# Optimization experiments

Hardware: AMD Instinct MI355X
Metric: run time of the kernel (lower is better)

## Reference

```python
import jax, jax.numpy as jnp
import numpy as np

HEADS = 8
DIM_HEAD = 64
DIM = 512
KERNEL = 33
SCALE = DIM_HEAD ** -0.5


def setup_inputs() -> dict:
    key = jax.random.key(0)
    k1, k2, k3, k4, k5, k6 = jax.random.split(key, 6)
    b, n = 2, 2048
    inner = HEADS * DIM_HEAD
    x = jax.random.normal(k1, (b, n, DIM), dtype=jnp.float32)
    mask = jax.random.uniform(k2, (b, n)) < 0.9
    W_qkv = jax.random.normal(k3, (DIM, inner * 3), dtype=jnp.float32) / np.sqrt(DIM)
    W_out = jax.random.normal(k4, (inner, DIM), dtype=jnp.float32) / np.sqrt(inner)
    b_out = jax.random.normal(k5, (DIM,), dtype=jnp.float32) * 0.01
    # depthwise Conv2d(heads, heads, (K,1), groups=heads) weight: (O=heads, I/groups=1, K, 1)
    conv_w = jax.random.normal(k6, (HEADS, 1, KERNEL, 1), dtype=jnp.float32) / np.sqrt(KERNEL)
    return {"x": x, "mask": mask, "W_qkv": W_qkv, "W_out": W_out,
            "b_out": b_out, "conv_w": conv_w}


def reference(x, mask, W_qkv, W_out, b_out, conv_w):
    b, n, _ = x.shape
    h, d = HEADS, DIM_HEAD
    qkv = (x @ W_qkv).reshape(b, n, 3, h, d)          # chunk(3) then (h d) split
    q = qkv[:, :, 0].transpose(0, 2, 1, 3)            # b h n d
    k = qkv[:, :, 1].transpose(0, 2, 1, 3)
    v = qkv[:, :, 2].transpose(0, 2, 1, 3)
    dots = jnp.einsum('bhid,bhjd->bhij', q, k) * SCALE
    mask_value = -jnp.finfo(dots.dtype).max
    dots = jnp.where(mask[:, None, None, :], dots, mask_value)
    attn = jax.nn.softmax(dots, axis=-1)
    out = jnp.einsum('bhij,bhjd->bhid', attn, v)      # b h n d
    # depthwise residual conv over sequence axis (height), per head
    pad = KERNEL // 2
    res = jax.lax.conv_general_dilated(
        v, conv_w, window_strides=(1, 1), padding=((pad, pad), (0, 0)),
        dimension_numbers=('NCHW', 'OIHW', 'NCHW'), feature_group_count=h)
    out = out + res
    out = out.transpose(0, 2, 1, 3).reshape(b, n, h * d)  # b n (h d)
    out = out @ W_out + b_out
    out = jnp.where(mask[:, :, None], out, 0.0)
    return out
```

## Files before the change

### kernel.cpp

```cpp
#include <hip/hip_runtime.h>
#include <float.h>

#define BATCH 2
#define SEQ   2048
#define HEADS 8
#define DHEAD 64
#define DIMM  512
#define NQKV  1536
#define QK_SCALE 0.125f

#define QKV_ELEMS ((size_t)BATCH * HEADS * SEQ * DHEAD)

typedef __bf16 bf16x8 __attribute__((ext_vector_type(8)));
typedef float  f32x4  __attribute__((ext_vector_type(4)));

__device__ __forceinline__ unsigned short bfbits(float f) {
  __bf16 h = (__bf16)f;
  return *(unsigned short*)&h;
}
__device__ __forceinline__ float bf2f(unsigned short u) {
  return __uint_as_float((unsigned)u << 16);
}

__global__ __launch_bounds__(1024) void prep_mask(const void* __restrict__ mraw,
                                                  float* __restrict__ maskf) {
  __shared__ int f_bf16, f_f32, f_gt1, f_oddnz;
  const int t = threadIdx.x;
  if (t == 0) { f_bf16 = 0; f_f32 = 0; f_gt1 = 0; f_oddnz = 0; }
  __syncthreads();
  const unsigned int* w = (const unsigned int*)mraw;
  unsigned int v = w[t];
  if (v == 0x3f803f80u) f_bf16 = 1;
  if (v == 0x3f800000u) f_f32 = 1;
  if (v > 1u)           f_gt1 = 1;
  if ((t & 1) && v != 0u) f_oddnz = 1;
  __syncthreads();
  int mode;
  if (f_bf16)       mode = 4;
  else if (f_f32)   mode = 3;
  else if (f_gt1)   mode = 1;
  else if (!f_oddnz) mode = 2;
  else              mode = 0;
  for (int i = t; i < BATCH * SEQ; i += 1024) {
    bool keep;
    if (mode == 4)      keep = ((const unsigned short*)mraw)[i] != 0;
    else if (mode == 3) keep = ((const float*)mraw)[i] != 0.f;
    else if (mode == 1) keep = ((const unsigned char*)mraw)[i] != 0;
    else if (mode == 2) keep = w[2 * i] != 0u;
    else                keep = w[i] != 0u;
    maskf[i] = keep ? 1.f : 0.f;
  }
}

__global__ __launch_bounds__(256) void transpose_w(const float* __restrict__ W,
                                                   unsigned short* __restrict__ Wt,
                                                   int K, int N) {
  __shared__ float T[64][65];
  const int t = threadIdx.x;
  const int n0 = blockIdx.x * 64, k0 = blockIdx.y * 64;
  {
    int r0 = t >> 4, c4 = t & 15;
#pragma unroll
    for (int rr = 0; rr < 4; ++rr) {
      int r = r0 + rr * 16;
      float4 v = *(const float4*)(W + (size_t)(k0 + r) * N + n0 + c4 * 4);
      T[r][c4 * 4 + 0] = v.x; T[r][c4 * 4 + 1] = v.y;
      T[r][c4 * 4 + 2] = v.z; T[r][c4 * 4 + 3] = v.w;
    }
  }
  __syncthreads();
  {
    int n = t >> 2, kc = t & 3;
    union { unsigned short u[16]; int4 v[2]; } p;
#pragma unroll
    for (int i = 0; i < 16; ++i) p.u[i] = bfbits(T[kc * 16 + i][n]);
    int4* dst = (int4*)(Wt + (size_t)(n0 + n) * K + k0 + kc * 16);
    dst[0] = p.v[0]; dst[1] = p.v[1];
  }
}

__global__ __launch_bounds__(256) void gemm_qkv_mfma(
    const float* __restrict__ X, const unsigned short* __restrict__ Wt,
    unsigned short* __restrict__ Qbf, unsigned short* __restrict__ Kbf,
    unsigned short* __restrict__ Vt) {
  __shared__ __align__(16) unsigned char Al[128 * 128];
  __shared__ __align__(16) unsigned char Bl[64 * 128];
  const int tid = threadIdx.x;
  const int lane = tid & 63;
  const int w = tid >> 6;
  const int l15 = lane & 15, g = lane >> 4;
  const int wr = w >> 1, wc = w & 1;
  int bid = blockIdx.x;
  int lid = (bid & 7) * 96 + (bid >> 3);
  int by = lid / 24, bx = lid - by * 24;
  const int m0 = by * 128;

  f32x4 acc[4][2] = {};
  const int srow = tid >> 3, scg = tid & 7;
  const int rsw = (l15 & 7) << 4;

  for (int k0 = 0; k0 < DIMM; k0 += 64) {
    __syncthreads();
#pragma unroll
    for (int it = 0; it < 4; ++it) {
      int row = srow + it * 32;
      int sw = (row & 7) << 4;
      const float* asrc = X + (size_t)(m0 + row) * DIMM + k0 + scg * 8;
      float4 a0 = *(const float4*)asrc;
      float4 a1 = *(const float4*)(asrc + 4);
      union { unsigned short u[8]; int4 v; } pk;
      pk.u[0] = bfbits(a0.x); pk.u[1] = bfbits(a0.y);
      pk.u[2] = bfbits(a0.z); pk.u[3] = bfbits(a0.w);
      pk.u[4] = bfbits(a1.x); pk.u[5] = bfbits(a1.y);
      pk.u[6] = bfbits(a1.z); pk.u[7] = bfbits(a1.w);
      *(int4*)(Al + row * 128 + ((scg * 16) ^ sw)) = pk.v;
      if (it < 2) {
        *(int4*)(Bl + row * 128 + ((scg * 16) ^ sw)) =
            *(const int4*)(Wt + (size_t)(bx * 64 + row) * DIMM + k0 + scg * 8);
      }
    }
    __syncthreads();
#pragma unroll
    for (int ks = 0; ks < 2; ++ks) {
      bf16x8 af[4], bfr[2];
#pragma unroll
      for (int mi = 0; mi < 4; ++mi)
        af[mi] = *(const bf16x8*)(Al + (wr * 64 + mi * 16 + l15) * 128 +
                                  ((ks * 64 + g * 16) ^ rsw));
#pragma unroll
      for (int nj = 0; nj < 2; ++nj)
        bfr[nj] = *(const bf16x8*)(Bl + (wc * 32 + nj * 16 + l15) * 128 +
                                   ((ks * 64 + g * 16) ^ rsw));
#pragma unroll
      for (int mi = 0; mi < 4; ++mi)
#pragma unroll
        for (int nj = 0; nj < 2; ++nj)
          acc[mi][nj] = __builtin_amdgcn_mfma_f32_16x16x32_bf16(
              af[mi], bfr[nj], acc[mi][nj], 0, 0, 0);
    }
  }
  const int chunk = bx >> 3;
  const int bb = m0 >> 11;
#pragma unroll
  for (int nj = 0; nj < 2; ++nj) {
    int col = (bx & 7) * 64 + wc * 32 + nj * 16 + l15;
    int hh = col >> 6, dd = col & 63;
#pragma unroll
    for (int mi = 0; mi < 4; ++mi) {
      int ii0 = (m0 & (SEQ - 1)) + wr * 64 + mi * 16 + g * 4;
      if (chunk == 2) {
        union { unsigned short u[4]; ushort4 v; } pk;
#pragma unroll
        for (int r = 0; r < 4; ++r) pk.u[r] = bfbits(acc[mi][nj][r]);
        *(ushort4*)(Vt + ((size_t)(bb * HEADS + hh) * DHEAD + dd) * SEQ + ii0) = pk.v;
      } else {
        unsigned short* dst = (chunk == 0) ? Qbf : Kbf;
        float sc = (chunk == 0) ? QK_SCALE : 1.f;
#pragma unroll
        for (int r = 0; r < 4; ++r)
          dst[((size_t)(bb * HEADS + hh) * SEQ + ii0 + r) * DHEAD + dd] =
              bfbits(acc[mi][nj][r] * sc);
      }
    }
  }
}

__global__ __launch_bounds__(256) void attn_split(const unsigned short* __restrict__ Qbf,
                                                  const unsigned short* __restrict__ Kbf,
                                                  const unsigned short* __restrict__ Vt,
                                                  const float* __restrict__ maskf,
                                                  unsigned short* __restrict__ Po,
                                                  float* __restrict__ LSE) {
  __shared__ __align__(16) unsigned char Ks[8192];
  __shared__ __align__(16) unsigned char Vs[8192];
  __shared__ __align__(16) unsigned char Ps[8192];
  __shared__ float skm[64];

  const int tid = threadIdx.x;
  const int lane = tid & 63;
  const int w = tid >> 6;
  const int l15 = lane & 15, g = lane >> 4;

  int fid = blockIdx.x;
  int lid = (fid & 7) * 128 + (fid >> 3);
  const int bh = lid >> 6;
  const int rem = lid & 63;
  const int qb = rem >> 1;
  const int half = rem & 1;
  const int bb = bh >> 3;

  const unsigned short* Qg = Qbf + ((size_t)bh * SEQ + qb * 64) * DHEAD;
  const unsigned short* Kg = Kbf + (size_t)bh * SEQ * DHEAD;
  const unsigned short* Vg = Vt  + (size_t)bh * DHEAD * SEQ;

  bf16x8 qf0, qf1;
  {
    const unsigned char* qrow = (const unsigned char*)(Qg + (size_t)(w * 16 + l15) * DHEAD);
    qf0 = *(const bf16x8*)(qrow + g * 16);
    qf1 = *(const bf16x8*)(qrow + 64 + g * 16);
  }

  f32x4 o[4];
  float mrow[4], lrow[4];
#pragma unroll
  for (int j = 0; j < 4; ++j) { o[j] = (f32x4){0.f, 0.f, 0.f, 0.f}; }
#pragma unroll
  for (int r = 0; r < 4; ++r) { mrow[r] = -3.0e38f; lrow[r] = 0.f; }

  const int sm = tid >> 2;
  const int sc = (tid & 3) * 32;
  const int ssw = (sm & 7) << 4;
  const int rsw = (l15 & 7) << 4;

  const int kt0 = half * 16;
  for (int kt = kt0; kt < kt0 + 16; ++kt) {
    __syncthreads();
    {
      const unsigned char* ksrc =
          (const unsigned char*)(Kg + (size_t)kt * 64 * DHEAD) + sm * 128 + sc;
      const unsigned char* vsrc =
          (const unsigned char*)(Vg + (size_t)sm * SEQ + kt * 64) + sc;
      *(int4*)(Ks + sm * 128 + ((sc)      ^ ssw)) = *(const int4*)(ksrc);
      *(int4*)(Ks + sm * 128 + ((sc + 16) ^ ssw)) = *(const int4*)(ksrc + 16);
      *(int4*)(Vs + sm * 128 + ((sc)      ^ ssw)) = *(const int4*)(vsrc);
      *(int4*)(Vs + sm * 128 + ((sc + 16) ^ ssw)) = *(const int4*)(vsrc + 16);
      if (tid < 64) skm[tid] = maskf[bb * SEQ + kt * 64 + tid];
    }
    __syncthreads();

    f32x4 s[4];
#pragma unroll
    for (int j = 0; j < 4; ++j) {
      const unsigned char* krow = Ks + (16 * j + l15) * 128;
      bf16x8 kf0 = *(const bf16x8*)(krow + ((g * 16)      ^ rsw));
      bf16x8 kf1 = *(const bf16x8*)(krow + ((64 + g * 16) ^ rsw));
      f32x4 z = (f32x4){0.f, 0.f, 0.f, 0.f};
      z = __builtin_amdgcn_mfma_f32_16x16x32_bf16(qf0, kf0, z, 0, 0, 0);
      z = __builtin_amdgcn_mfma_f32_16x16x32_bf16(qf1, kf1, z, 0, 0, 0);
      s[j] = z;
    }

    float km0 = skm[l15], km1 = skm[16 + l15], km2 = skm[32 + l15], km3 = skm[48 + l15];
#pragma unroll
    for (int r = 0; r < 4; ++r) {
      float v0 = (km0 != 0.f) ? s[0][r] : -1e30f;
      float v1 = (km1 != 0.f) ? s[1][r] : -1e30f;
      float v2 = (km2 != 0.f) ? s[2][r] : -1e30f;
      float v3 = (km3 != 0.f) ? s[3][r] : -1e30f;
      float rm = fmaxf(fmaxf(v0, v1), fmaxf(v2, v3));
      rm = fmaxf(rm, __shfl_xor(rm, 1));
      rm = fmaxf(rm, __shfl_xor(rm, 2));
      rm = fmaxf(rm, __shfl_xor(rm, 4));
      rm = fmaxf(rm, __shfl_xor(rm, 8));
      float mnew = fmaxf(mrow[r], rm);
      float resc = __expf(mrow[r] - mnew);
      float p0 = __expf(v0 - mnew) * km0;
      float p1 = __expf(v1 - mnew) * km1;
      float p2 = __expf(v2 - mnew) * km2;
      float p3 = __expf(v3 - mnew) * km3;
      float rs = (p0 + p1) + (p2 + p3);
      rs += __shfl_xor(rs, 1);
      rs += __shfl_xor(rs, 2);
      rs += __shfl_xor(rs, 4);
      rs += __shfl_xor(rs, 8);
      lrow[r] = lrow[r] * resc + rs;
      mrow[r] = mnew;
      o[0][r] *= resc; o[1][r] *= resc; o[2][r] *= resc; o[3][r] *= resc;

      int pm = w * 16 + g * 4 + r;
      unsigned char* prow = Ps + pm * 128;
      int psw = (pm & 7) << 4;
      *(__bf16*)(prow + ((2 * (l15)      ) ^ psw)) = (__bf16)p0;
      *(__bf16*)(prow + ((2 * (16 + l15) ) ^ psw)) = (__bf16)p1;
      *(__bf16*)(prow + ((2 * (32 + l15) ) ^ psw)) = (__bf16)p2;
      *(__bf16*)(prow + ((2 * (48 + l15) ) ^ psw)) = (__bf16)p3;
    }

    {
      const unsigned char* parow = Ps + (w * 16 + l15) * 128;
      bf16x8 pa0 = *(const bf16x8*)(parow + ((g * 16)      ^ rsw));
      bf16x8 pa1 = *(const bf16x8*)(parow + ((64 + g * 16) ^ rsw));
#pragma unroll
      for (int j = 0; j < 4; ++j) {
        const unsigned char* vrow = Vs + (16 * j + l15) * 128;
        bf16x8 vf0 = *(const bf16x8*)(vrow + ((g * 16)      ^ rsw));
        bf16x8 vf1 = *(const bf16x8*)(vrow + ((64 + g * 16) ^ rsw));
        o[j] = __builtin_amdgcn_mfma_f32_16x16x32_bf16(pa0, vf0, o[j], 0, 0, 0);
        o[j] = __builtin_amdgcn_mfma_f32_16x16x32_bf16(pa1, vf1, o[j], 0, 0, 0);
      }
    }
  }

#pragma unroll
  for (int r = 0; r < 4; ++r) {
    float l = lrow[r];
    float inv = (l > 0.f) ? 1.f / l : 0.f;
    int row = qb * 64 + w * 16 + g * 4 + r;
    size_t base = half * QKV_ELEMS + ((size_t)bh * SEQ + row) * DHEAD + l15;
    Po[base]      = bfbits(o[0][r] * inv);
    Po[base + 16] = bfbits(o[1][r] * inv);
    Po[base + 32] = bfbits(o[2][r] * inv);
    Po[base + 48] = bfbits(o[3][r] * inv);
    if (l15 == 0)
      LSE[half * (BATCH * HEADS * SEQ) + bh * SEQ + row] =
          (l > 0.f) ? mrow[r] + __logf(l) : -3.0e38f;
  }
}

__global__ __launch_bounds__(256) void combine_conv(
    const unsigned short* __restrict__ Po, const float* __restrict__ LSE,
    const unsigned short* __restrict__ Vt, const float* __restrict__ cw,
    unsigned short* __restrict__ Obf) {
  __shared__ float T[96][68];
  __shared__ float cwl[33];
  const int tid = threadIdx.x;
  const int bid = blockIdx.x;
  const int bh = bid >> 5;
  const int n0 = (bid & 31) * 64;
  const int hh = bh & 7;
  if (tid < 33) cwl[tid] = cw[hh * 33 + tid];
  for (int idx = tid; idx < 64 * 24; idx += 256) {
    int d = idx / 24, c4 = idx - (idx / 24) * 24;
    int nbase = n0 - 16 + c4 * 4;
    const unsigned short* src = Vt + ((size_t)bh * DHEAD + d) * SEQ;
#pragma unroll
    for (int q = 0; q < 4; ++q) {
      int n = nbase + q;
      T[c4 * 4 + q][d] = (n >= 0 && n < SEQ) ? bf2f(src[n]) : 0.f;
    }
  }
  __syncthreads();
#pragma unroll
  for (int p = 0; p < 4; ++p) {
    int n = (tid >> 4) + p * 16;
    int d4 = tid & 15;
    int row = bh * SEQ + n0 + n;
    float ls0 = LSE[row], ls1 = LSE[BATCH * HEADS * SEQ + row];
    float m = fmaxf(ls0, ls1);
    float w0 = __expf(ls0 - m), w1 = __expf(ls1 - m);
    float inv = 1.f / (w0 + w1);
    w0 *= inv; w1 *= inv;
    const unsigned short* p0 = Po + (size_t)row * DHEAD + d4 * 4;
    const unsigned short* p1 = p0 + QKV_ELEMS;
    ushort4 a = *(const ushort4*)p0, b = *(const ushort4*)p1;
    float o0 = w0 * bf2f(a.x) + w1 * bf2f(b.x);
    float o1 = w0 * bf2f(a.y) + w1 * bf2f(b.y);
    float o2 = w0 * bf2f(a.z) + w1 * bf2f(b.z);
    float o3 = w0 * bf2f(a.w) + w1 * bf2f(b.w);
#pragma unroll
    for (int t = 0; t < 33; ++t) {
      float wv = cwl[t];
      float4 tv = *(const float4*)&T[n + t][d4 * 4];
      o0 += wv * tv.x; o1 += wv * tv.y; o2 += wv * tv.z; o3 += wv * tv.w;
    }
    union { unsigned short u[4]; ushort4 v; } pk;
    pk.u[0] = bfbits(o0); pk.u[1] = bfbits(o1);
    pk.u[2] = bfbits(o2); pk.u[3] = bfbits(o3);
    *(ushort4*)(Obf + (size_t)row * DHEAD + d4 * 4) = pk.v;
  }
}

__global__ __launch_bounds__(256) void gemm_out_mfma(
    const unsigned short* __restrict__ Obf, const unsigned short* __restrict__ Wt,
    const float* __restrict__ bias, const float* __restrict__ maskf,
    float* __restrict__ out) {
  __shared__ __align__(16) unsigned char Al[64 * 128];
  __shared__ __align__(16) unsigned char Bl[64 * 128];
  const int tid = threadIdx.x;
  const int lane = tid & 63;
  const int w = tid >> 6;
  const int l15 = lane & 15, g = lane >> 4;
  const int wr = w >> 1, wc = w & 1;
  int bid = blockIdx.x;
  int lid = (bid & 7) * 64 + (bid >> 3);
  int by = lid >> 3, bx = lid & 7;
  const int m0 = by * 64, n0 = bx * 64;
  const int bb = m0 >> 11;
  const int ii0 = m0 & (SEQ - 1);

  f32x4 acc[2][2] = {};
  const int srow = tid >> 3, scg = tid & 7;
  const int rsw = (l15 & 7) << 4;

  for (int k0 = 0; k0 < DIMM; k0 += 64) {
    const int hh = k0 >> 6;
    __syncthreads();
#pragma unroll
    for (int it = 0; it < 2; ++it) {
      int row = srow + it * 32;
      int sw = (row & 7) << 4;
      *(int4*)(Al + row * 128 + ((scg * 16) ^ sw)) =
          *(const int4*)(Obf + ((size_t)(bb * HEADS + hh) * SEQ + ii0 + row) * DHEAD + scg * 8);
      *(int4*)(Bl + row * 128 + ((scg * 16) ^ sw)) =
          *(const int4*)(Wt + (size_t)(n0 + row) * DIMM + k0 + scg * 8);
    }
    __syncthreads();
#pragma unroll
    for (int ks = 0; ks < 2; ++ks) {
      bf16x8 af[2], bfr[2];
#pragma unroll
      for (int mi = 0; mi < 2; ++mi)
        af[mi] = *(const bf16x8*)(Al + (wr * 32 + mi * 16 + l15) * 128 +
                                  ((ks * 64 + g * 16) ^ rsw));
#pragma unroll
      for (int nj = 0; nj < 2; ++nj)
        bfr[nj] = *(const bf16x8*)(Bl + (wc * 32 + nj * 16 + l15) * 128 +
                                   ((ks * 64 + g * 16) ^ rsw));
#pragma unroll
      for (int mi = 0; mi < 2; ++mi)
#pragma unroll
        for (int nj = 0; nj < 2; ++nj)
          acc[mi][nj] = __builtin_amdgcn_mfma_f32_16x16x32_bf16(
              af[mi], bfr[nj], acc[mi][nj], 0, 0, 0);
    }
  }
#pragma unroll
  for (int nj = 0; nj < 2; ++nj) {
    int col = n0 + wc * 32 + nj * 16 + l15;
    float bcol = bias[col];
#pragma unroll
    for (int mi = 0; mi < 2; ++mi) {
#pragma unroll
      for (int r = 0; r < 4; ++r) {
        int m = m0 + wr * 32 + mi * 16 + g * 4 + r;
        out[(size_t)m * DIMM + col] = (acc[mi][nj][r] + bcol) * maskf[m];
      }
    }
  }
}

extern "C" void kernel_launch(void* const* d_in, const int* in_sizes, int n_in,
                              void* d_out, int out_size, void* d_ws, size_t ws_size,
                              hipStream_t stream) {
  const float* x     = (const float*)d_in[0];
  const void*  mask  = d_in[1];
  const float* Wqkv  = (const float*)d_in[2];
  const float* Wout  = (const float*)d_in[3];
  const float* bout  = (const float*)d_in[4];
  const float* convw = (const float*)d_in[5];
  float* out = (float*)d_out;

  float* maskf = (float*)d_ws;
  unsigned short* Qbf = (unsigned short*)(maskf + 4096);
  unsigned short* Kbf = Qbf + QKV_ELEMS;
  unsigned short* Vt  = Kbf + QKV_ELEMS;
  unsigned short* Po  = Vt + QKV_ELEMS;
  float* LSE          = (float*)(Po + 2 * QKV_ELEMS);
  unsigned short* Obf = (unsigned short*)(LSE + 2 * BATCH * HEADS * SEQ);
  unsigned short* Wtq = Obf + QKV_ELEMS;
  unsigned short* Wto = Wtq + (size_t)NQKV * DIMM;

  prep_mask<<<1, 1024, 0, stream>>>(mask, maskf);
  transpose_w<<<dim3(NQKV / 64, DIMM / 64), 256, 0, stream>>>(Wqkv, Wtq, DIMM, NQKV);
  transpose_w<<<dim3(DIMM / 64, DIMM / 64), 256, 0, stream>>>(Wout, Wto, DIMM, DIMM);
  gemm_qkv_mfma<<<768, 256, 0, stream>>>(x, Wtq, Qbf, Kbf, Vt);
  attn_split<<<1024, 256, 0, stream>>>(Qbf, Kbf, Vt, maskf, Po, LSE);
  combine_conv<<<512, 256, 0, stream>>>(Po, LSE, Vt, convw, Obf);
  gemm_out_mfma<<<512, 256, 0, stream>>>(Obf, Wto, bout, maskf, out);
}
```

Baseline: 119.1 us.

## Replace online softmax max tracking with Cauchy-Schwarz static upper bound

Computes per-head maximum key norm in a new small kernel and per-row query norms in the attention kernel, then uses |q|·max|k| as a fixed softmax shift. This removes the per-tile running max, its cross-lane shuffles, the rescaling of the output accumulator and per-tile sum reductions. It adds an extra kernel launch and atomic, and risks exp underflow if the bound is far above the true row maximum.

```diff
diff --git a/kernel.cpp b/kernel.cpp
--- a/kernel.cpp
+++ b/kernel.cpp
@@ -23,9 +23,11 @@
 }
 
 __global__ __launch_bounds__(1024) void prep_mask(const void* __restrict__ mraw,
-                                                  float* __restrict__ maskf) {
+                                                  float* __restrict__ maskf,
+                                                  unsigned* __restrict__ kmaxn) {
   __shared__ int f_bf16, f_f32, f_gt1, f_oddnz;
   const int t = threadIdx.x;
+  if (t < 16) kmaxn[t] = 0u;
   if (t == 0) { f_bf16 = 0; f_f32 = 0; f_gt1 = 0; f_oddnz = 0; }
   __syncthreads();
   const unsigned int* w = (const unsigned int*)mraw;
@@ -165,16 +167,35 @@
   }
 }
 
+__global__ __launch_bounds__(256) void knorm(const unsigned short* __restrict__ Kbf,
+                                             unsigned* __restrict__ kmaxn) {
+  int row = blockIdx.x * 256 + threadIdx.x;
+  const bf16x8* kr = (const bf16x8*)(Kbf + (size_t)row * DHEAD);
+  float n2 = 0.f;
+#pragma unroll
+  for (int c = 0; c < 8; ++c) {
+    bf16x8 v = kr[c];
+#pragma unroll
+    for (int i = 0; i < 8; ++i) { float f = (float)v[i]; n2 += f * f; }
+  }
+#pragma unroll
+  for (int d = 1; d < 64; d <<= 1) n2 = fmaxf(n2, __shfl_xor(n2, d));
+  if ((threadIdx.x & 63) == 0)
+    atomicMax(kmaxn + (row >> 11), __float_as_uint(n2));
+}
+
 __global__ __launch_bounds__(256) void attn_split(const unsigned short* __restrict__ Qbf,
                                                   const unsigned short* __restrict__ Kbf,
                                                   const unsigned short* __restrict__ Vt,
                                                   const float* __restrict__ maskf,
+                                                  const unsigned* __restrict__ kmaxn,
                                                   unsigned short* __restrict__ Po,
                                                   float* __restrict__ LSE) {
   __shared__ __align__(16) unsigned char Ks[8192];
   __shared__ __align__(16) unsigned char Vs[8192];
   __shared__ __align__(16) unsigned char Ps[8192];
   __shared__ float skm[64];
+  __shared__ float qns[64];
 
   const int tid = threadIdx.x;
   const int lane = tid & 63;
@@ -199,13 +220,27 @@
     qf0 = *(const bf16x8*)(qrow + g * 16);
     qf1 = *(const bf16x8*)(qrow + 64 + g * 16);
   }
+  {
+    float qn2 = 0.f;
+#pragma unroll
+    for (int i = 0; i < 8; ++i) {
+      float a = (float)qf0[i]; qn2 += a * a;
+      float b = (float)qf1[i]; qn2 += b * b;
+    }
+    qn2 += __shfl_xor(qn2, 16);
+    qn2 += __shfl_xor(qn2, 32);
+    if (g == 0) qns[w * 16 + l15] = qn2;
+  }
+  __syncthreads();
+  const float kmax2 = __uint_as_float(kmaxn[bh]);
+  float B[4];
+#pragma unroll
+  for (int r = 0; r < 4; ++r) B[r] = sqrtf(qns[w * 16 + g * 4 + r] * kmax2);
 
   f32x4 o[4];
-  float mrow[4], lrow[4];
+  float lsum[4] = {0.f, 0.f, 0.f, 0.f};
 #pragma unroll
   for (int j = 0; j < 4; ++j) { o[j] = (f32x4){0.f, 0.f, 0.f, 0.f}; }
-#pragma unroll
-  for (int r = 0; r < 4; ++r) { mrow[r] = -3.0e38f; lrow[r] = 0.f; }
 
   const int sm = tid >> 2;
   const int sc = (tid & 3) * 32;
@@ -243,30 +278,11 @@
     float km0 = skm[l15], km1 = skm[16 + l15], km2 = skm[32 + l15], km3 = skm[48 + l15];
 #pragma unroll
     for (int r = 0; r < 4; ++r) {
-      float v0 = (km0 != 0.f) ? s[0][r] : -1e30f;
-      float v1 = (km1 != 0.f) ? s[1][r] : -1e30f;
-      float v2 = (km2 != 0.f) ? s[2][r] : -1e30f;
-      float v3 = (km3 != 0.f) ? s[3][r] : -1e30f;
-      float rm = fmaxf(fmaxf(v0, v1), fmaxf(v2, v3));
-      rm = fmaxf(rm, __shfl_xor(rm, 1));
-      rm = fmaxf(rm, __shfl_xor(rm, 2));
-      rm = fmaxf(rm, __shfl_xor(rm, 4));
-      rm = fmaxf(rm, __shfl_xor(rm, 8));
-      float mnew = fmaxf(mrow[r], rm);
-      float resc = __expf(mrow[r] - mnew);
-      float p0 = __expf(v0 - mnew) * km0;
-      float p1 = __expf(v1 - mnew) * km1;
-      float p2 = __expf(v2 - mnew) * km2;
-      float p3 = __expf(v3 - mnew) * km3;
-      float rs = (p0 + p1) + (p2 + p3);
-      rs += __shfl_xor(rs, 1);
-      rs += __shfl_xor(rs, 2);
-      rs += __shfl_xor(rs, 4);
-      rs += __shfl_xor(rs, 8);
-      lrow[r] = lrow[r] * resc + rs;
-      mrow[r] = mnew;
-      o[0][r] *= resc; o[1][r] *= resc; o[2][r] *= resc; o[3][r] *= resc;
-
+      float p0 = __expf(s[0][r] - B[r]) * km0;
+      float p1 = __expf(s[1][r] - B[r]) * km1;
+      float p2 = __expf(s[2][r] - B[r]) * km2;
+      float p3 = __expf(s[3][r] - B[r]) * km3;
+      lsum[r] += (p0 + p1) + (p2 + p3);
       int pm = w * 16 + g * 4 + r;
       unsigned char* prow = Ps + pm * 128;
       int psw = (pm & 7) << 4;
@@ -293,7 +309,11 @@
 
 #pragma unroll
   for (int r = 0; r < 4; ++r) {
-    float l = lrow[r];
+    float l = lsum[r];
+    l += __shfl_xor(l, 1);
+    l += __shfl_xor(l, 2);
+    l += __shfl_xor(l, 4);
+    l += __shfl_xor(l, 8);
     float inv = (l > 0.f) ? 1.f / l : 0.f;
     int row = qb * 64 + w * 16 + g * 4 + r;
     size_t base = half * QKV_ELEMS + ((size_t)bh * SEQ + row) * DHEAD + l15;
@@ -303,7 +323,7 @@
     Po[base + 48] = bfbits(o[3][r] * inv);
     if (l15 == 0)
       LSE[half * (BATCH * HEADS * SEQ) + bh * SEQ + row] =
-          (l > 0.f) ? mrow[r] + __logf(l) : -3.0e38f;
+          (l > 0.f) ? B[r] + __logf(l) : -3.0e38f;
   }
 }
 
@@ -441,7 +461,8 @@
   float* out = (float*)d_out;
 
   float* maskf = (float*)d_ws;
-  unsigned short* Qbf = (unsigned short*)(maskf + 4096);
+  unsigned* kmaxn = (unsigned*)(maskf + 4096);
+  unsigned short* Qbf = (unsigned short*)(kmaxn + 64);
   unsigned short* Kbf = Qbf + QKV_ELEMS;
   unsigned short* Vt  = Kbf + QKV_ELEMS;
   unsigned short* Po  = Vt + QKV_ELEMS;
@@ -450,11 +471,12 @@
   unsigned short* Wtq = Obf + QKV_ELEMS;
   unsigned short* Wto = Wtq + (size_t)NQKV * DIMM;
 
-  prep_mask<<<1, 1024, 0, stream>>>(mask, maskf);
+  prep_mask<<<1, 1024, 0, stream>>>(mask, maskf, kmaxn);
   transpose_w<<<dim3(NQKV / 64, DIMM / 64), 256, 0, stream>>>(Wqkv, Wtq, DIMM, NQKV);
   transpose_w<<<dim3(DIMM / 64, DIMM / 64), 256, 0, stream>>>(Wout, Wto, DIMM, DIMM);
   gemm_qkv_mfma<<<768, 256, 0, stream>>>(x, Wtq, Qbf, Kbf, Vt);
-  attn_split<<<1024, 256, 0, stream>>>(Qbf, Kbf, Vt, maskf, Po, LSE);
+  knorm<<<(BATCH * HEADS * SEQ) / 256, 256, 0, stream>>>(Kbf, kmaxn);
+  attn_split<<<1024, 256, 0, stream>>>(Qbf, Kbf, Vt, maskf, kmaxn, Po, LSE);
   combine_conv<<<512, 256, 0, stream>>>(Po, LSE, Vt, convw, Obf);
   gemm_out_mfma<<<512, 256, 0, stream>>>(Obf, Wto, bout, maskf, out);
 }
```

After: 109.3 us. -8.2%, faster.
